# Optimization experiments

Measured on AMD Instinct MI355X. Metric: run time of the kernel, lower is better.

Reference implementation:

```python
import jax, jax.numpy as jnp
import numpy as np


def _make_kernels():
    k3 = jnp.array([[0, 1, 0], [1, -4, 1], [0, 1, 0]], dtype=jnp.float32)
    k3 = jnp.tile(k3[None, None], (4, 1, 1, 1))  # [4,1,3,3] depthwise OIHW
    k5 = jnp.array([[0, 0, -1, 0, 0],
                    [0, -1, -2, -1, 0],
                    [-1, -2, 16, -2, -1],
                    [0, -1, -2, -1, 0],
                    [0, 0, -1, 0, 0]], dtype=jnp.float32)
    k5 = jnp.tile(k5[None, None], (4, 1, 1, 1))  # [4,1,5,5]
    return k3, k5


def setup_inputs() -> dict:
    key = jax.random.key(0)
    x = jax.random.normal(key, (32, 4, 512, 512), dtype=jnp.float32)
    k3, k5 = _make_kernels()
    return {"x": x, "k3": k3, "k5": k5}


def _dwconv(x, k, pad):
    # depthwise conv: groups == in_channels == 4
    return jax.lax.conv_general_dilated(
        x, k,
        window_strides=(1, 1),
        padding=((pad, pad), (pad, pad)),
        dimension_numbers=("NCHW", "OIHW", "NCHW"),
        feature_group_count=4,
    )


def reference(x, k3, k5):
    e3 = _dwconv(x, k3, 1)                 # [B,4,H,W]
    e5 = _dwconv(x, k5, 2)                 # [B,4,H,W]
    response = jnp.maximum(jnp.abs(e3), jnp.abs(e5))
    edge_map = jnp.max(response, axis=1, keepdims=True)  # [B,1,H,W]
    v_min = jnp.min(edge_map, axis=(1, 2, 3), keepdims=True)
    v_max = jnp.max(edge_map, axis=(1, 2, 3), keepdims=True)
    return (edge_map - v_min) / (v_max - v_min + 1e-6)
```

## Files before the change

kernel.cpp:

```cpp
#include <hip/hip_runtime.h>

#define IH 512
#define IW 512
#define NC 4
#define NB 32
#define RPT 4
#define NTILES 2048
#define TW 140
#define TROWS 36
#define CPR 35
#define NCHUNK (CPR * TROWS)

typedef float v4f __attribute__((ext_vector_type(4)));

__device__ __attribute__((aligned(16))) const float ZEROPAGE[4] = {0.f, 0.f, 0.f, 0.f};

typedef const __attribute__((address_space(1))) void gvoid_t;
typedef __attribute__((address_space(3))) void svoid_t;

__device__ __forceinline__ void stage_tile(const float* __restrict__ xc,
                                           float* __restrict__ lbuf,
                                           int R0, int C0, int wv, int ln) {
    const int bases[5] = {0, 256, 512, 768, NCHUNK - 256};
    #pragma unroll
    for (int rno = 0; rno < 5; ++rno) {
        const int chunk = bases[rno] + wv * 64 + ln;
        const int row   = chunk / CPR;
        const int blk   = chunk - row * CPR;
        const int gr    = R0 - 2 + row;
        const int gc    = C0 - 4 + blk * 4;
        const bool valid = (gr >= 0) & (gr < IH) & (gc >= 0) & (gc + 4 <= IW);
        const float* src = valid ? (xc + (size_t)gr * IW + gc) : ZEROPAGE;
        float* ldst = lbuf + (size_t)(bases[rno] + wv * 64) * 4;
        __builtin_amdgcn_global_load_lds((gvoid_t*)src, (svoid_t*)ldst, 16, 0, 0);
    }
}

__device__ __forceinline__ void load_wrow(const float* __restrict__ lds,
                                          int Lr, int qx, float* __restrict__ d) {
    const float* p = lds + Lr * TW + qx * 4 + 2;
    float2 a  = *(const float2*)(p + 0);
    float2 b  = *(const float2*)(p + 2);
    float2 c  = *(const float2*)(p + 4);
    float2 dd = *(const float2*)(p + 6);
    d[0] = a.x;  d[1] = a.y;  d[2] = b.x;  d[3] = b.y;
    d[4] = c.x;  d[5] = c.y;  d[6] = dd.x; d[7] = dd.y;
}

__device__ __forceinline__ void stencil_row(const float* __restrict__ rm2,
                                            const float* __restrict__ rm1,
                                            const float* __restrict__ r0c,
                                            const float* __restrict__ rp1,
                                            const float* __restrict__ rp2,
                                            float* __restrict__ acc) {
    #pragma unroll
    for (int j = 0; j < 4; ++j) {
        const int i = 2 + j;
        const float c0     = r0c[i];
        const float cross1 = rm1[i] + rp1[i] + r0c[i - 1] + r0c[i + 1];
        const float e3     = cross1 - 4.f * c0;
        const float ring   = rm2[i] + rp2[i] + r0c[i - 2] + r0c[i + 2]
                           + rm1[i - 1] + rm1[i + 1]
                           + rp1[i - 1] + rp1[i + 1];
        const float e5     = 16.f * c0 - 2.f * cross1 - ring;
        const float rc     = fmaxf(fabsf(e3), fabsf(e5));
        acc[j] = fmaxf(acc[j], rc);
    }
}

__global__ __launch_bounds__(256, 4) void edge_tiled(
        const float* __restrict__ x, float* __restrict__ out,
        float* __restrict__ slotmin, float* __restrict__ slotmax) {
    __shared__ float lds[NCHUNK * 4];
    __shared__ float smin[4], smax[4];

    const int qx  = threadIdx.x & 31;
    const int tyg = (threadIdx.x >> 5) & 7;
    const int wv  = threadIdx.x >> 6;
    const int ln  = threadIdx.x & 63;
    const int C0  = blockIdx.x * 128;
    const int R0  = blockIdx.y * 32;
    const int b   = blockIdx.z;

    const float* xb = x + (size_t)b * NC * IH * IW;

    float resp[RPT][4];
    #pragma unroll
    for (int k = 0; k < RPT; ++k)
        #pragma unroll
        for (int j = 0; j < 4; ++j) resp[k][j] = 0.f;

    #pragma unroll 1
    for (int c = 0; c < NC; ++c) {
        stage_tile(xb + (size_t)c * IH * IW, lds, R0, C0, wv, ln);
        __syncthreads();

        const int r0 = tyg * 4;
        float w0[8], w1[8], w2[8], w3[8], w4[8];
        load_wrow(lds, r0 + 0, qx, w0);
        load_wrow(lds, r0 + 1, qx, w1);
        load_wrow(lds, r0 + 2, qx, w2);
        load_wrow(lds, r0 + 3, qx, w3);
        load_wrow(lds, r0 + 4, qx, w4);
        stencil_row(w0, w1, w2, w3, w4, resp[0]);
        load_wrow(lds, r0 + 5, qx, w0);
        stencil_row(w1, w2, w3, w4, w0, resp[1]);
        load_wrow(lds, r0 + 6, qx, w1);
        stencil_row(w2, w3, w4, w0, w1, resp[2]);
        load_wrow(lds, r0 + 7, qx, w2);
        stencil_row(w3, w4, w0, w1, w2, resp[3]);

        __syncthreads();
    }

    const int w     = C0 + qx * 4;
    const int hbase = R0 + tyg * 4;
    float* ob = out + ((size_t)b * IH + hbase) * IW + w;
    #pragma unroll
    for (int k = 0; k < RPT; ++k) {
        float4 o;
        o.x = resp[k][0]; o.y = resp[k][1]; o.z = resp[k][2]; o.w = resp[k][3];
        *(float4*)(ob + (size_t)k * IW) = o;
    }

    float lmin = resp[0][0], lmax = resp[0][0];
    #pragma unroll
    for (int k = 0; k < RPT; ++k)
        #pragma unroll
        for (int j = 0; j < 4; ++j) {
            lmin = fminf(lmin, resp[k][j]);
            lmax = fmaxf(lmax, resp[k][j]);
        }
    #pragma unroll
    for (int off = 32; off >= 1; off >>= 1) {
        lmin = fminf(lmin, __shfl_down(lmin, off));
        lmax = fmaxf(lmax, __shfl_down(lmax, off));
    }
    if (ln == 0) { smin[wv] = lmin; smax[wv] = lmax; }
    __syncthreads();
    if (threadIdx.x == 0) {
        const float m0 = fminf(fminf(smin[0], smin[1]), fminf(smin[2], smin[3]));
        const float M0 = fmaxf(fmaxf(smax[0], smax[1]), fmaxf(smax[2], smax[3]));
        const int slot = b * 64 + blockIdx.y * 4 + blockIdx.x;
        slotmin[slot] = m0;
        slotmax[slot] = M0;
    }
}

__global__ __launch_bounds__(256) void norm_tile(
        float* __restrict__ out,
        const float* __restrict__ slotmin,
        const float* __restrict__ slotmax) {
    const int qx    = threadIdx.x & 31;
    const int tyg   = threadIdx.x >> 5;
    const int w     = blockIdx.x * 128 + qx * 4;
    const int hbase = blockIdx.y * (8 * RPT) + tyg * RPT;
    const int b     = blockIdx.z;

    __shared__ float sv[2];
    if (threadIdx.x < 64) {
        float mn = slotmin[b * 64 + threadIdx.x];
        float mx = slotmax[b * 64 + threadIdx.x];
        #pragma unroll
        for (int off = 32; off >= 1; off >>= 1) {
            mn = fminf(mn, __shfl_down(mn, off));
            mx = fmaxf(mx, __shfl_down(mx, off));
        }
        if (threadIdx.x == 0) { sv[0] = mn; sv[1] = mx; }
    }
    __syncthreads();
    const float vmin = sv[0];
    const float inv  = 1.0f / (sv[1] - vmin + 1e-6f);

    float* ob = out + ((size_t)b * IH + hbase) * IW + w;
    #pragma unroll
    for (int k = 0; k < RPT; ++k) {
        const float4 u = *(const float4*)(ob + (size_t)k * IW);
        v4f o;
        o.x = (u.x - vmin) * inv;
        o.y = (u.y - vmin) * inv;
        o.z = (u.z - vmin) * inv;
        o.w = (u.w - vmin) * inv;
        __builtin_nontemporal_store(o, (v4f*)(ob + (size_t)k * IW));
    }
}

extern "C" void kernel_launch(void* const* d_in, const int* in_sizes, int n_in,
                              void* d_out, int out_size, void* d_ws, size_t ws_size,
                              hipStream_t stream) {
    const float* x = (const float*)d_in[0];
    float* out = (float*)d_out;
    float* slotmin = (float*)d_ws;
    float* slotmax = slotmin + NTILES;

    hipLaunchKernelGGL(edge_tiled, dim3(4, 16, NB), dim3(256), 0, stream,
                       x, out, slotmin, slotmax);
    hipLaunchKernelGGL(norm_tile, dim3(4, 16, NB), dim3(256), 0, stream,
                       out, slotmin, slotmax);
}
```

Before: 214.3 us.

## Double-buffer LDS channel tiles to overlap async loads with stencil compute

The edge kernel now has two LDS tile buffers. While the stencil runs on channel c from one buffer, the async global_load_lds for channel c+1 is issued into the other. The channel loop is fully unrolled and the first tile is staged before the loop, which removes one barrier-and-wait per channel. The cost is double the LDS per block (about 40 KB), which leaves very little headroom for 4 blocks per CU.

```diff
diff --git a/kernel.cpp b/kernel.cpp
--- a/kernel.cpp
+++ b/kernel.cpp
@@ -10,6 +10,7 @@
 #define TROWS 36
 #define CPR 35
 #define NCHUNK (CPR * TROWS)
+#define BUFSZ (NCHUNK * 4)
 
 typedef float v4f __attribute__((ext_vector_type(4)));
 
@@ -36,9 +37,9 @@
     }
 }
 
-__device__ __forceinline__ void load_wrow(const float* __restrict__ lds,
+__device__ __forceinline__ void load_wrow(const float* __restrict__ lds_,
                                           int Lr, int qx, float* __restrict__ d) {
-    const float* p = lds + Lr * TW + qx * 4 + 2;
+    const float* p = lds_ + Lr * TW + qx * 4 + 2;
     float2 a  = *(const float2*)(p + 0);
     float2 b  = *(const float2*)(p + 2);
     float2 c  = *(const float2*)(p + 4);
@@ -68,10 +69,29 @@
     }
 }
 
+__device__ __forceinline__ void compute_chan(const float* __restrict__ buf,
+                                             int tyg, int qx,
+                                             float (&resp)[RPT][4]) {
+    const int r0 = tyg * 4;
+    float w0[8], w1[8], w2[8], w3[8], w4[8];
+    load_wrow(buf, r0 + 0, qx, w0);
+    load_wrow(buf, r0 + 1, qx, w1);
+    load_wrow(buf, r0 + 2, qx, w2);
+    load_wrow(buf, r0 + 3, qx, w3);
+    load_wrow(buf, r0 + 4, qx, w4);
+    stencil_row(w0, w1, w2, w3, w4, resp[0]);
+    load_wrow(buf, r0 + 5, qx, w0);
+    stencil_row(w1, w2, w3, w4, w0, resp[1]);
+    load_wrow(buf, r0 + 6, qx, w1);
+    stencil_row(w2, w3, w4, w0, w1, resp[2]);
+    load_wrow(buf, r0 + 7, qx, w2);
+    stencil_row(w3, w4, w0, w1, w2, resp[3]);
+}
+
 __global__ __launch_bounds__(256, 4) void edge_tiled(
         const float* __restrict__ x, float* __restrict__ out,
         float* __restrict__ slotmin, float* __restrict__ slotmax) {
-    __shared__ float lds[NCHUNK * 4];
+    __shared__ float lds[2 * BUFSZ];
     __shared__ float smin[4], smax[4];
 
     const int qx  = threadIdx.x & 31;
@@ -90,26 +110,16 @@
         #pragma unroll
         for (int j = 0; j < 4; ++j) resp[k][j] = 0.f;
 
-    #pragma unroll 1
+    stage_tile(xb, lds, R0, C0, wv, ln);
+    __syncthreads();
+
+    #pragma unroll
     for (int c = 0; c < NC; ++c) {
-        stage_tile(xb + (size_t)c * IH * IW, lds, R0, C0, wv, ln);
-        __syncthreads();
-
-        const int r0 = tyg * 4;
-        float w0[8], w1[8], w2[8], w3[8], w4[8];
-        load_wrow(lds, r0 + 0, qx, w0);
-        load_wrow(lds, r0 + 1, qx, w1);
-        load_wrow(lds, r0 + 2, qx, w2);
-        load_wrow(lds, r0 + 3, qx, w3);
-        load_wrow(lds, r0 + 4, qx, w4);
-        stencil_row(w0, w1, w2, w3, w4, resp[0]);
-        load_wrow(lds, r0 + 5, qx, w0);
-        stencil_row(w1, w2, w3, w4, w0, resp[1]);
-        load_wrow(lds, r0 + 6, qx, w1);
-        stencil_row(w2, w3, w4, w0, w1, resp[2]);
-        load_wrow(lds, r0 + 7, qx, w2);
-        stencil_row(w3, w4, w0, w1, w2, resp[3]);
-
+        float* cur = lds + (c & 1) * BUFSZ;
+        float* nxt = lds + ((c + 1) & 1) * BUFSZ;
+        if (c + 1 < NC)
+            stage_tile(xb + (size_t)(c + 1) * IH * IW, nxt, R0, C0, wv, ln);
+        compute_chan(cur, tyg, qx, resp);
         __syncthreads();
     }
 
```

Result: no change. 214.1 us (-0.1%).
